# Kernel optimization log

Hardware: AMD Instinct MI355X
Metric: run time of the kernel (lower is better)

The kernel has to match this reference:

```python
import jax, jax.numpy as jnp
import numpy as np

B, S, D, H = 2, 2048, 1024, 16
DK = D // H
NEG = -1.0e9


def setup_inputs() -> dict:
    key = jax.random.key(0)
    ks = jax.random.split(key, 11)
    inp = {
        "q": jax.random.normal(ks[0], (B, S, D), jnp.float32),
        "k": jax.random.normal(ks[1], (B, S, D), jnp.float32),
        "v": jax.random.normal(ks[2], (B, S, D), jnp.float32),
        "mask": jnp.tril(jnp.ones((S, S), jnp.int32))[None, None],  # causal [1,1,S,S]
    }
    scale = 0.02
    inp["w_q"] = jax.random.normal(ks[3], (D, D), jnp.float32) * scale
    inp["b_q"] = jnp.zeros((D,), jnp.float32)
    inp["w_k"] = jax.random.normal(ks[4], (D, D), jnp.float32) * scale
    inp["b_k"] = jnp.zeros((D,), jnp.float32)
    inp["w_v"] = jax.random.normal(ks[5], (D, D), jnp.float32) * scale
    inp["b_v"] = jnp.zeros((D,), jnp.float32)
    inp["w_o"] = jax.random.normal(ks[6], (D, D), jnp.float32) * scale
    inp["b_o"] = jnp.zeros((D,), jnp.float32)
    return inp


def reference(q, k, v, mask, w_q, b_q, w_k, b_k, w_v, b_v, w_o, b_o):
    # projections: [B,S,D] -> [B,H,S,DK]
    def proj(x, w, b):
        y = jnp.einsum("bsd,de->bse", x, w) + b
        return y.reshape(B, S, H, DK).transpose(0, 2, 1, 3)

    Q = proj(q, w_q, b_q)
    K = proj(k, w_k, b_k)
    V = proj(v, w_v, b_v)
    # explicit scores matrix, faithful to the original naive attention
    scores = jnp.einsum("bhsd,bhtd->bhst", Q, K) / jnp.sqrt(jnp.float32(DK))
    scores = jnp.where(mask == 0, NEG, scores)
    attn = jax.nn.softmax(scores, axis=-1)  # dropout p=0.0 -> identity
    x = jnp.einsum("bhst,bhtd->bhsd", attn, V)
    x = x.transpose(0, 2, 1, 3).reshape(B, S, D)
    return jnp.einsum("bsd,de->bse", x, w_o) + b_o
```

## Files before the change

kernel.cpp:

```cpp
#include <hip/hip_runtime.h>
#include <hip/hip_bf16.h>

typedef __bf16 bf16;
typedef __bf16 bf16x2 __attribute__((ext_vector_type(2)));
typedef __bf16 bf16x8 __attribute__((ext_vector_type(8)));
typedef float f32x4 __attribute__((ext_vector_type(4)));

#define MFMA16(a, b, c) __builtin_amdgcn_mfma_f32_16x16x32_bf16(a, b, c, 0, 0, 0)

#define QSCALE 0.18033688f

#define GLOAD_LDS(g, l)                                              \
  __builtin_amdgcn_global_load_lds(                                  \
      (const __attribute__((address_space(1))) void*)(g),            \
      (__attribute__((address_space(3))) void*)(l), 16, 0, 0)

__global__ __launch_bounds__(256) void convert_k(const float* __restrict__ q,
                                                 const float* __restrict__ k,
                                                 const float* __restrict__ v,
                                                 bf16* __restrict__ qb,
                                                 bf16* __restrict__ kb,
                                                 bf16* __restrict__ vb) {
  const float* src = blockIdx.y == 0 ? q : blockIdx.y == 1 ? k : v;
  bf16* dst = blockIdx.y == 0 ? qb : blockIdx.y == 1 ? kb : vb;
  const size_t i = ((size_t)blockIdx.x * 256 + threadIdx.x) * 8;
  float4 a = *(const float4*)(src + i);
  float4 b = *(const float4*)(src + i + 4);
  bf16x8 o;
  o[0] = (bf16)a.x; o[1] = (bf16)a.y; o[2] = (bf16)a.z; o[3] = (bf16)a.w;
  o[4] = (bf16)b.x; o[5] = (bf16)b.y; o[6] = (bf16)b.z; o[7] = (bf16)b.w;
  *(bf16x8*)(dst + i) = o;
}

__global__ __launch_bounds__(256) void transpose_w(const float* __restrict__ w0,
                                                   const float* __restrict__ w1,
                                                   const float* __restrict__ w2,
                                                   const float* __restrict__ w3,
                                                   bf16* __restrict__ dst) {
  __shared__ bf16 T[64][68];
  const float* W = blockIdx.z == 0 ? w0 : blockIdx.z == 1 ? w1
                   : blockIdx.z == 2 ? w2 : w3;
  bf16* Y = dst + (size_t)blockIdx.z * 1024 * 1024;
  const int t = threadIdx.x, r = t >> 2, c4 = t & 3;
  const int k0 = blockIdx.y * 64, n0 = blockIdx.x * 64;

  const float4* src = (const float4*)(W + (size_t)(k0 + r) * 1024 + n0 + c4 * 16);
  float4 f0 = src[0], f1 = src[1], f2 = src[2], f3 = src[3];
  bf16* row = &T[r][c4 * 16];
  row[0] = (bf16)f0.x; row[1] = (bf16)f0.y; row[2] = (bf16)f0.z; row[3] = (bf16)f0.w;
  row[4] = (bf16)f1.x; row[5] = (bf16)f1.y; row[6] = (bf16)f1.z; row[7] = (bf16)f1.w;
  row[8] = (bf16)f2.x; row[9] = (bf16)f2.y; row[10] = (bf16)f2.z; row[11] = (bf16)f2.w;
  row[12] = (bf16)f3.x; row[13] = (bf16)f3.y; row[14] = (bf16)f3.z; row[15] = (bf16)f3.w;
  __syncthreads();

  bf16x8 o0, o1;
#pragma unroll
  for (int j = 0; j < 8; ++j) o0[j] = T[c4 * 16 + j][r];
#pragma unroll
  for (int j = 0; j < 8; ++j) o1[j] = T[c4 * 16 + 8 + j][r];
  bf16* d = Y + (size_t)(n0 + r) * 1024 + k0 + c4 * 16;
  *(bf16x8*)d = o0;
  *(bf16x8*)(d + 8) = o1;
}

template <int QKV>
__global__ __launch_bounds__(256) void gemm128(
    const bf16* __restrict__ xq, const bf16* __restrict__ xk,
    const bf16* __restrict__ xv, const bf16* __restrict__ Wt,
    const float* __restrict__ bq, const float* __restrict__ bk,
    const float* __restrict__ bv, bf16* __restrict__ Qp,
    bf16* __restrict__ Kp, bf16* __restrict__ Vtp, float* __restrict__ Yf) {
  __shared__ bf16 Al[128 * 32];
  __shared__ bf16 Bl[128 * 32];

  const int z = QKV ? blockIdx.z : 0;
  const bf16* X = QKV ? (z == 0 ? xq : z == 1 ? xk : xv) : xq;
  const bf16* Bt = Wt + (size_t)z * 1048576;
  const float* bias = QKV ? (z == 0 ? bq : z == 1 ? bk : bv) : bq;
  const float escale = (QKV && z == 0) ? QSCALE : 1.0f;

  const int t = threadIdx.x;
  const int wave = t >> 6, lane = t & 63, quad = lane >> 4, l16 = lane & 15;
  const int wm = (wave >> 1) * 64, wn = (wave & 1) * 64;
  const int bm = blockIdx.y * 128, bn = blockIdx.x * 128;

  const int off = wave * 1024 + lane * 16;
  const int srow = off >> 6;
  const int scol = (off & 63) >> 1;
  const bf16* gA0 = X + (size_t)(bm + srow) * 1024 + scol;
  const bf16* gA1 = X + (size_t)(bm + 64 + srow) * 1024 + scol;
  const bf16* gB0 = Bt + (size_t)(bn + srow) * 1024 + scol;
  const bf16* gB1 = Bt + (size_t)(bn + 64 + srow) * 1024 + scol;
  bf16* ldsA0 = Al + wave * 512;
  bf16* ldsA1 = Al + 2048 + wave * 512;
  bf16* ldsB0 = Bl + wave * 512;
  bf16* ldsB1 = Bl + 2048 + wave * 512;

  f32x4 acc[4][4] = {};

  for (int kb = 0; kb < 1024; kb += 32) {
    GLOAD_LDS(gA0 + kb, ldsA0);
    GLOAD_LDS(gA1 + kb, ldsA1);
    GLOAD_LDS(gB0 + kb, ldsB0);
    GLOAD_LDS(gB1 + kb, ldsB1);
    __syncthreads();

    bf16x8 af[4], bfr[4];
#pragma unroll
    for (int mt = 0; mt < 4; ++mt)
      af[mt] = *(const bf16x8*)(Al + (wm + mt * 16 + l16) * 32 + quad * 8);
#pragma unroll
    for (int nt = 0; nt < 4; ++nt)
      bfr[nt] = *(const bf16x8*)(Bl + (wn + nt * 16 + l16) * 32 + quad * 8);
#pragma unroll
    for (int mt = 0; mt < 4; ++mt)
#pragma unroll
      for (int nt = 0; nt < 4; ++nt)
        acc[mt][nt] = MFMA16(af[mt], bfr[nt], acc[mt][nt]);
    __syncthreads();
  }

#pragma unroll
  for (int mt = 0; mt < 4; ++mt)
#pragma unroll
    for (int nt = 0; nt < 4; ++nt) {
      const int gn = bn + wn + nt * 16 + l16;
      const float bia = bias[gn];
#pragma unroll
      for (int r = 0; r < 4; ++r) {
        const int gm = bm + wm + mt * 16 + quad * 4 + r;
        const float val = (acc[mt][nt][r] + bia) * escale;
        if (!QKV) {
          Yf[(size_t)gm * 1024 + gn] = val;
        } else {
          const int b = gm >> 11, s = gm & 2047;
          const int h = gn >> 6, dk = gn & 63;
          if (z <= 1) {
            bf16* Y = (z == 0) ? Qp : Kp;
            Y[((size_t)(b * 16 + h) * 2048 + s) * 64 + dk] = (bf16)val;
          } else {
            Vtp[((size_t)(b * 16 + h) * 64 + dk) * 2048 + s] = (bf16)val;
          }
        }
      }
    }
}

__global__ __launch_bounds__(256) void attn_k(const bf16* __restrict__ Q,
                                              const bf16* __restrict__ K,
                                              const bf16* __restrict__ Vt,
                                              bf16* __restrict__ X) {
  __shared__ bf16 Kl[64 * 72];
  __shared__ bf16 Vl[64 * 72];
  __shared__ bf16 Pb[4][16 * 72];

  const int t = threadIdx.x;
  const int wave = t >> 6, lane = t & 63, quad = lane >> 4, l16 = lane & 15;
  const int pairx = blockIdx.x, bh = blockIdx.y;
  const int b = bh >> 4, h = bh & 15;

  const bf16* Qb = Q + (size_t)bh * 2048 * 64;
  const bf16* Kb = K + (size_t)bh * 2048 * 64;
  const bf16* Vb = Vt + (size_t)bh * 64 * 2048;

  const int srow = t >> 2;
  const int scol = (t & 3) * 16;

  bf16x8 onesf;
#pragma unroll
  for (int i = 0; i < 8; ++i) onesf[i] = (bf16)1.0f;

  bf16* Pw = Pb[wave];

  for (int phase = 0; phase < 2; ++phase) {
    const int qtile = phase ? (31 - pairx) : pairx;
    const int ntiles = qtile + 1;
    const int q0 = qtile * 64 + wave * 16;

    bf16x8 qf0 = *(const bf16x8*)(Qb + (q0 + l16) * 64 + quad * 8);
    bf16x8 qf1 = *(const bf16x8*)(Qb + (q0 + l16) * 64 + 32 + quad * 8);

    f32x4 o[4] = {};
    f32x4 o4 = {};

    {
      const bf16* kp = Kb + srow * 64 + scol;
      const bf16* vp = Vb + (size_t)srow * 2048 + scol;
      bf16x8 k0r = *(const bf16x8*)kp;
      bf16x8 k1r = *(const bf16x8*)(kp + 8);
      bf16x8 v0r = *(const bf16x8*)vp;
      bf16x8 v1r = *(const bf16x8*)(vp + 8);
      *(bf16x8*)(Kl + srow * 72 + scol) = k0r;
      *(bf16x8*)(Kl + srow * 72 + scol + 8) = k1r;
      *(bf16x8*)(Vl + srow * 72 + scol) = v0r;
      *(bf16x8*)(Vl + srow * 72 + scol + 8) = v1r;
    }
    __syncthreads();

    for (int kt = 0; kt < ntiles; ++kt) {
      const int k0 = kt * 64;
      const bool more = (kt + 1) < ntiles;
      bf16x8 kr0, kr1, vr0, vr1;
      if (more) {
        const bf16* kp = Kb + (k0 + 64 + srow) * 64 + scol;
        const bf16* vp = Vb + (size_t)srow * 2048 + k0 + 64 + scol;
        kr0 = *(const bf16x8*)kp;
        kr1 = *(const bf16x8*)(kp + 8);
        vr0 = *(const bf16x8*)vp;
        vr1 = *(const bf16x8*)(vp + 8);
      }

      f32x4 sc[4];
#pragma unroll
      for (int nt = 0; nt < 4; ++nt) {
        bf16x8 kf0 = *(const bf16x8*)(Kl + (nt * 16 + l16) * 72 + quad * 8);
        bf16x8 kf1 = *(const bf16x8*)(Kl + (nt * 16 + l16) * 72 + 32 + quad * 8);
        f32x4 s = {};
        s = MFMA16(qf0, kf0, s);
        s = MFMA16(qf1, kf1, s);
        sc[nt] = s;
      }

#pragma unroll
      for (int r = 0; r < 4; ++r) {
        const int row = quad * 4 + r;
        const int qg = q0 + row;
#pragma unroll
        for (int nt = 0; nt < 4; ++nt) {
          const int key = k0 + nt * 16 + l16;
          const float p = (key <= qg) ? exp2f(sc[nt][r]) : 0.f;
          Pw[row * 72 + nt * 16 + l16] = (bf16)p;
        }
      }
      __builtin_amdgcn_s_waitcnt(0xC07F);

      bf16x8 pf0 = *(const bf16x8*)(Pw + l16 * 72 + quad * 8);
      bf16x8 pf1 = *(const bf16x8*)(Pw + l16 * 72 + 32 + quad * 8);
      o4 = MFMA16(pf0, onesf, o4);
      o4 = MFMA16(pf1, onesf, o4);
#pragma unroll
      for (int dt = 0; dt < 4; ++dt) {
        bf16x8 vf0 = *(const bf16x8*)(Vl + (dt * 16 + l16) * 72 + quad * 8);
        bf16x8 vf1 = *(const bf16x8*)(Vl + (dt * 16 + l16) * 72 + 32 + quad * 8);
        o[dt] = MFMA16(pf0, vf0, o[dt]);
        o[dt] = MFMA16(pf1, vf1, o[dt]);
      }

      __syncthreads();
      if (more) {
        *(bf16x8*)(Kl + srow * 72 + scol) = kr0;
        *(bf16x8*)(Kl + srow * 72 + scol + 8) = kr1;
        *(bf16x8*)(Vl + srow * 72 + scol) = vr0;
        *(bf16x8*)(Vl + srow * 72 + scol + 8) = vr1;
        __syncthreads();
      }
    }

#pragma unroll
    for (int r = 0; r < 4; ++r) {
      const float rinv = 1.0f / o4[r];
      const int qg = q0 + quad * 4 + r;
#pragma unroll
      for (int dt = 0; dt < 4; ++dt) {
        const int col = h * 64 + dt * 16 + l16;
        X[((size_t)b * 2048 + qg) * 1024 + col] = (bf16)(o[dt][r] * rinv);
      }
    }
    __syncthreads();
  }
}

extern "C" void kernel_launch(void* const* d_in, const int* in_sizes, int n_in,
                              void* d_out, int out_size, void* d_ws,
                              size_t ws_size, hipStream_t stream) {
  const float* q = (const float*)d_in[0];
  const float* k = (const float*)d_in[1];
  const float* v = (const float*)d_in[2];
  const float* w_q = (const float*)d_in[4];
  const float* b_q = (const float*)d_in[5];
  const float* w_k = (const float*)d_in[6];
  const float* b_k = (const float*)d_in[7];
  const float* w_v = (const float*)d_in[8];
  const float* b_v = (const float*)d_in[9];
  const float* w_o = (const float*)d_in[10];
  const float* b_o = (const float*)d_in[11];

  bf16* ws = (bf16*)d_ws;
  const size_t NELEM = (size_t)4096 * 1024;
  bf16* Qp = ws;
  bf16* Kp = ws + NELEM;
  bf16* Vtp = ws + 2 * NELEM;
  bf16* Xp = ws + 3 * NELEM;
  bf16* Wt = ws + 4 * NELEM;
  bf16* Wto = Wt + 3145728;
  bf16* qb = Xp;
  bf16* kb = (bf16*)d_out;
  bf16* vb = kb + NELEM;

  convert_k<<<dim3(2048, 3), 256, 0, stream>>>(q, k, v, qb, kb, vb);
  transpose_w<<<dim3(16, 16, 4), 256, 0, stream>>>(w_q, w_k, w_v, w_o, Wt);

  gemm128<1><<<dim3(8, 32, 3), 256, 0, stream>>>(qb, kb, vb, Wt, b_q, b_k, b_v,
                                                 Qp, Kp, Vtp, nullptr);
  attn_k<<<dim3(16, 32), 256, 0, stream>>>(Qp, Kp, Vtp, Xp);
  gemm128<0><<<dim3(8, 32), 256, 0, stream>>>(Xp, nullptr, nullptr, Wto, b_o,
                                              nullptr, nullptr, nullptr,
                                              nullptr, nullptr, (float*)d_out);
}
```

Measured before the change: 256.4 us.

## Stage V-projection transpose through LDS and halve output GEMM M-tile

The V projection epilogue now writes each tile into a shared-memory buffer and then emits the transposed Vt rows as contiguous 16-byte vector stores, replacing scattered 2-byte strided stores. The output projection GEMM is templated to a 64-row M tile, which doubles its grid to 512 blocks so more compute units have work. The costs are an extra LDS buffer and barriers in the V epilogue, plus lower operand reuse per block in the output GEMM.

Result: no change. 261.0 us (+1.8%).

```diff
diff --git a/kernel.cpp b/kernel.cpp
--- a/kernel.cpp
+++ b/kernel.cpp
@@ -63,14 +63,14 @@
   *(bf16x8*)(d + 8) = o1;
 }
 
-template <int QKV>
+template <int QKV, int MT>
 __global__ __launch_bounds__(256) void gemm128(
     const bf16* __restrict__ xq, const bf16* __restrict__ xk,
     const bf16* __restrict__ xv, const bf16* __restrict__ Wt,
     const float* __restrict__ bq, const float* __restrict__ bk,
     const float* __restrict__ bv, bf16* __restrict__ Qp,
     bf16* __restrict__ Kp, bf16* __restrict__ Vtp, float* __restrict__ Yf) {
-  __shared__ bf16 Al[128 * 32];
+  __shared__ bf16 Al[MT * 32 * 32];
   __shared__ bf16 Bl[128 * 32];
 
   const int z = QKV ? blockIdx.z : 0;
@@ -81,8 +81,8 @@
 
   const int t = threadIdx.x;
   const int wave = t >> 6, lane = t & 63, quad = lane >> 4, l16 = lane & 15;
-  const int wm = (wave >> 1) * 64, wn = (wave & 1) * 64;
-  const int bm = blockIdx.y * 128, bn = blockIdx.x * 128;
+  const int wm = (wave >> 1) * (MT * 16), wn = (wave & 1) * 64;
+  const int bm = blockIdx.y * (MT * 32), bn = blockIdx.x * 128;
 
   const int off = wave * 1024 + lane * 16;
   const int srow = off >> 6;
@@ -96,54 +96,85 @@
   bf16* ldsB0 = Bl + wave * 512;
   bf16* ldsB1 = Bl + 2048 + wave * 512;
 
-  f32x4 acc[4][4] = {};
+  f32x4 acc[MT][4] = {};
 
   for (int kb = 0; kb < 1024; kb += 32) {
     GLOAD_LDS(gA0 + kb, ldsA0);
-    GLOAD_LDS(gA1 + kb, ldsA1);
+    if (MT == 4) GLOAD_LDS(gA1 + kb, ldsA1);
     GLOAD_LDS(gB0 + kb, ldsB0);
     GLOAD_LDS(gB1 + kb, ldsB1);
     __syncthreads();
 
-    bf16x8 af[4], bfr[4];
-#pragma unroll
-    for (int mt = 0; mt < 4; ++mt)
+    bf16x8 af[MT], bfr[4];
+#pragma unroll
+    for (int mt = 0; mt < MT; ++mt)
       af[mt] = *(const bf16x8*)(Al + (wm + mt * 16 + l16) * 32 + quad * 8);
 #pragma unroll
     for (int nt = 0; nt < 4; ++nt)
       bfr[nt] = *(const bf16x8*)(Bl + (wn + nt * 16 + l16) * 32 + quad * 8);
 #pragma unroll
-    for (int mt = 0; mt < 4; ++mt)
+    for (int mt = 0; mt < MT; ++mt)
 #pragma unroll
       for (int nt = 0; nt < 4; ++nt)
         acc[mt][nt] = MFMA16(af[mt], bfr[nt], acc[mt][nt]);
     __syncthreads();
   }
 
-#pragma unroll
-  for (int mt = 0; mt < 4; ++mt)
-#pragma unroll
-    for (int nt = 0; nt < 4; ++nt) {
-      const int gn = bn + wn + nt * 16 + l16;
-      const float bia = bias[gn];
-#pragma unroll
-      for (int r = 0; r < 4; ++r) {
-        const int gm = bm + wm + mt * 16 + quad * 4 + r;
-        const float val = (acc[mt][nt][r] + bia) * escale;
-        if (!QKV) {
-          Yf[(size_t)gm * 1024 + gn] = val;
-        } else {
-          const int b = gm >> 11, s = gm & 2047;
-          const int h = gn >> 6, dk = gn & 63;
-          if (z <= 1) {
+  if (QKV && z == 2) {
+    __shared__ bf16 Tt[64 * 136];
+    const int b = bm >> 11;
+#pragma unroll
+    for (int half = 0; half < 2; ++half) {
+      if ((wave & 1) == half) {
+#pragma unroll
+        for (int nt = 0; nt < 4; ++nt) {
+          const int ln = nt * 16 + l16;
+          const float bia = bias[bn + half * 64 + ln];
+#pragma unroll
+          for (int mt = 0; mt < 4; ++mt)
+#pragma unroll
+            for (int r = 0; r < 4; ++r) {
+              const int m = wm + mt * 16 + quad * 4 + r;
+              Tt[ln * 136 + m] = (bf16)(acc[mt][nt][r] + bia);
+            }
+        }
+      }
+      __syncthreads();
+      {
+        const int ln = t >> 2, seg = (t & 3) * 32;
+        const int gn = bn + half * 64 + ln;
+        const int h = gn >> 6, dk = gn & 63;
+        const int s0 = (bm & 2047) + seg;
+        bf16* dst = Vtp + ((size_t)(b * 16 + h) * 64 + dk) * 2048 + s0;
+        const bf16* srcp = Tt + ln * 136 + seg;
+#pragma unroll
+        for (int j = 0; j < 4; ++j)
+          *(bf16x8*)(dst + j * 8) = *(const bf16x8*)(srcp + j * 8);
+      }
+      __syncthreads();
+    }
+  } else {
+#pragma unroll
+    for (int mt = 0; mt < MT; ++mt)
+#pragma unroll
+      for (int nt = 0; nt < 4; ++nt) {
+        const int gn = bn + wn + nt * 16 + l16;
+        const float bia = bias[gn];
+#pragma unroll
+        for (int r = 0; r < 4; ++r) {
+          const int gm = bm + wm + mt * 16 + quad * 4 + r;
+          const float val = (acc[mt][nt][r] + bia) * escale;
+          if (!QKV) {
+            Yf[(size_t)gm * 1024 + gn] = val;
+          } else {
+            const int b = gm >> 11, s = gm & 2047;
+            const int h = gn >> 6, dk = gn & 63;
             bf16* Y = (z == 0) ? Qp : Kp;
             Y[((size_t)(b * 16 + h) * 2048 + s) * 64 + dk] = (bf16)val;
-          } else {
-            Vtp[((size_t)(b * 16 + h) * 64 + dk) * 2048 + s] = (bf16)val;
           }
         }
       }
-    }
+  }
 }
 
 __global__ __launch_bounds__(256) void attn_k(const bf16* __restrict__ Q,
@@ -300,10 +331,10 @@
   convert_k<<<dim3(2048, 3), 256, 0, stream>>>(q, k, v, qb, kb, vb);
   transpose_w<<<dim3(16, 16, 4), 256, 0, stream>>>(w_q, w_k, w_v, w_o, Wt);
 
-  gemm128<1><<<dim3(8, 32, 3), 256, 0, stream>>>(qb, kb, vb, Wt, b_q, b_k, b_v,
-                                                 Qp, Kp, Vtp, nullptr);
+  gemm128<1, 4><<<dim3(8, 32, 3), 256, 0, stream>>>(
+      qb, kb, vb, Wt, b_q, b_k, b_v, Qp, Kp, Vtp, nullptr);
   attn_k<<<dim3(16, 32), 256, 0, stream>>>(Qp, Kp, Vtp, Xp);
-  gemm128<0><<<dim3(8, 32), 256, 0, stream>>>(Xp, nullptr, nullptr, Wto, b_o,
-                                              nullptr, nullptr, nullptr,
-                                              nullptr, nullptr, (float*)d_out);
-}
+  gemm128<0, 2><<<dim3(8, 64), 256, 0, stream>>>(
+      Xp, nullptr, nullptr, Wto, b_o, nullptr, nullptr, nullptr, nullptr,
+      nullptr, (float*)d_out);
+}
```
